# Performance work log

Hardware: AMD Instinct MI355X
Metric: run time of the kernel (lower is better)

The kernel has to match this reference:

```python
import jax, jax.numpy as jnp
import numpy as np

L, B, T, C, H, V = 6, 8, 1024, 1024, 16, 4096
HS = C // H  # head size = 64


def _ln(x, g, b):
    mu = x.mean(-1, keepdims=True)
    var = ((x - mu) ** 2).mean(-1, keepdims=True)
    return (x - mu) * jax.lax.rsqrt(var + 1e-5) * g + b


def setup_inputs() -> dict:
    key = jax.random.key(0)
    ks = jax.random.split(key, 12)
    s = 0.02
    return {
        "idx": jax.random.randint(ks[0], (B, T), 0, V),
        "tok_emb": jax.random.normal(ks[1], (V, C), jnp.float32) * s,
        "pos_emb": jax.random.normal(ks[2], (T, C), jnp.float32) * s,
        "Wq": jax.random.normal(ks[3], (L, C, C), jnp.float32) * s,
        "Wk": jax.random.normal(ks[4], (L, C, C), jnp.float32) * s,
        "Wv": jax.random.normal(ks[5], (L, C, C), jnp.float32) * s,
        "Wo": jax.random.normal(ks[6], (L, C, C), jnp.float32) * s,
        "bo": jnp.zeros((L, C), jnp.float32),
        "ln1_g": jnp.ones((L, C), jnp.float32),
        "ln1_b": jnp.zeros((L, C), jnp.float32),
        "ln2_g": jnp.ones((L, C), jnp.float32),
        "ln2_b": jnp.zeros((L, C), jnp.float32),
        "W1": jax.random.normal(ks[7], (L, C, 4 * C), jnp.float32) * s,
        "b1": jnp.zeros((L, 4 * C), jnp.float32),
        "W2": jax.random.normal(ks[8], (L, 4 * C, C), jnp.float32) * s,
        "b2": jnp.zeros((L, C), jnp.float32),
        "lnf_g": jnp.ones((C,), jnp.float32),
        "lnf_b": jnp.zeros((C,), jnp.float32),
        "lm_w": jax.random.normal(ks[9], (C, V), jnp.float32) * s,
        "lm_b": jnp.zeros((V,), jnp.float32),
    }


def _gpt(idx, tok_emb, pos_emb, Wq, Wk, Wv, Wo, bo, ln1_g, ln1_b, ln2_g, ln2_b,
         W1, b1, W2, b2, lnf_g, lnf_b, lm_w, lm_b):
    x = tok_emb[idx] + pos_emb[None, :idx.shape[1]]  # (B,T,C)
    mask = jnp.tril(jnp.ones((T, T), bool))
    neg_inf = jnp.float32(-jnp.inf)

    def block(x, p):
        wq, wk, wv, wo, bo_, g1, be1, g2, be2, w1, bb1, w2, bb2 = p
        h = _ln(x, g1, be1)
        # per-head projections (no bias), heads concatenated along feature dim
        q = (h @ wq).reshape(B, T, H, HS)
        k = (h @ wk).reshape(B, T, H, HS)
        v = (h @ wv).reshape(B, T, H, HS)
        # NOTE: faithful to source -- scores are MULTIPLIED by sqrt(head_size)
        att = jnp.einsum('bqhd,bkhd->bhqk', q, k) * (HS ** 0.5)
        att = jnp.where(mask, att, neg_inf)
        p_att = jax.nn.softmax(att, axis=-1)  # dropout is identity at eval
        o = jnp.einsum('bhqk,bkhd->bqhd', p_att, v).reshape(B, T, C)
        x = x + o @ wo + bo_
        h2 = _ln(x, g2, be2)
        x = x + jax.nn.relu(h2 @ w1 + bb1) @ w2 + bb2
        return x, None

    x, _ = jax.lax.scan(
        block, x,
        (Wq, Wk, Wv, Wo, bo, ln1_g, ln1_b, ln2_g, ln2_b, W1, b1, W2, b2))
    x = _ln(x, lnf_g, lnf_b)
    return x @ lm_w + lm_b  # logits (B,T,V)


def reference(idx, tok_emb, pos_emb, Wq, Wk, Wv, Wo, bo, ln1_g, ln1_b, ln2_g,
              ln2_b, W1, b1, W2, b2, lnf_g, lnf_b, lm_w, lm_b):
    return _gpt(idx, tok_emb, pos_emb, Wq, Wk, Wv, Wo, bo, ln1_g, ln1_b,
                ln2_g, ln2_b, W1, b1, W2, b2, lnf_g, lnf_b, lm_w, lm_b)
```

## Files before the change

### kernel.cpp

```cpp
#include <hip/hip_runtime.h>

#define LL 6
#define BB 8
#define TT 1024
#define CC 1024
#define HH 16
#define HS 64
#define VV 4096
#define BT (BB*TT)

typedef __attribute__((ext_vector_type(4))) float f32x4;
typedef __attribute__((ext_vector_type(8))) short bf16x8;

__device__ __forceinline__ float bf2f(unsigned short u) {
  union { unsigned int u; float f; } v; v.u = ((unsigned int)u) << 16; return v.f;
}
__device__ __forceinline__ unsigned short rne16(float f) {
  unsigned u = __float_as_uint(f);
  return (unsigned short)((u + 0x7fffu + ((u >> 16) & 1u)) >> 16);
}
__device__ __forceinline__ void gld16(const uint4* g, uint4* l) {
  __builtin_amdgcn_global_load_lds(
      (const __attribute__((address_space(1))) void*)g,
      (__attribute__((address_space(3))) void*)l, 16, 0, 0);
}

__global__ __launch_bounds__(256) void embed_kernel(
    const int* __restrict__ idx, const float* __restrict__ tok,
    const float* __restrict__ pos, float* __restrict__ x) {
  int bt = blockIdx.x;
  int t = bt & (TT - 1);
  int id = idx[bt];
  float4 te = reinterpret_cast<const float4*>(tok)[(size_t)id * (CC/4) + threadIdx.x];
  float4 pe = reinterpret_cast<const float4*>(pos)[(size_t)t * (CC/4) + threadIdx.x];
  float4 r; r.x = te.x+pe.x; r.y = te.y+pe.y; r.z = te.z+pe.z; r.w = te.w+pe.w;
  reinterpret_cast<float4*>(x)[(size_t)bt * (CC/4) + threadIdx.x] = r;
}

struct Oct3 { uint4 p0, p1, p2; };
__device__ __forceinline__ unsigned pk2(unsigned lo, unsigned hi) {
  return (lo >> 16) | (hi & 0xffff0000u);
}
__device__ __forceinline__ Oct3 split8(const float* f) {
  unsigned a0[8], a1[8], a2[8];
  #pragma unroll
  for (int e = 0; e < 8; ++e) {
    float v = f[e];
    unsigned u = __float_as_uint(v);
    a0[e] = u;
    float r = v - __uint_as_float(u & 0xffff0000u);
    unsigned ur = __float_as_uint(r);
    a1[e] = ur;
    float r2 = r - __uint_as_float(ur & 0xffff0000u);
    a2[e] = __float_as_uint(r2);
  }
  Oct3 o;
  o.p0 = make_uint4(pk2(a0[0],a0[1]), pk2(a0[2],a0[3]), pk2(a0[4],a0[5]), pk2(a0[6],a0[7]));
  o.p1 = make_uint4(pk2(a1[0],a1[1]), pk2(a1[2],a1[3]), pk2(a1[4],a1[5]), pk2(a1[6],a1[7]));
  o.p2 = make_uint4(pk2(a2[0],a2[1]), pk2(a2[2],a2[3]), pk2(a2[4],a2[5]), pk2(a2[6],a2[7]));
  return o;
}
struct Oct2 { uint4 p0, p1; };
__device__ __forceinline__ Oct2 split8_rne2(const float* f) {
  unsigned h0[8], h1[8];
  #pragma unroll
  for (int e = 0; e < 8; ++e) {
    h0[e] = rne16(f[e]);
    float r = f[e] - bf2f((unsigned short)h0[e]);
    h1[e] = rne16(r);
  }
  Oct2 o;
  o.p0 = make_uint4(h0[0]|(h0[1]<<16), h0[2]|(h0[3]<<16), h0[4]|(h0[5]<<16), h0[6]|(h0[7]<<16));
  o.p1 = make_uint4(h1[0]|(h1[1]<<16), h1[2]|(h1[3]<<16), h1[4]|(h1[5]<<16), h1[6]|(h1[7]<<16));
  return o;
}
__device__ __forceinline__ uint4 pack8_rne(const float* f) {
  unsigned h[8];
  #pragma unroll
  for (int e = 0; e < 8; ++e) h[e] = rne16(f[e]);
  return make_uint4(h[0]|(h[1]<<16), h[2]|(h[3]<<16), h[4]|(h[5]<<16), h[6]|(h[7]<<16));
}

__global__ __launch_bounds__(256) void ln32_kernel(
    const float* __restrict__ x, const float* __restrict__ g,
    const float* __restrict__ b, float* __restrict__ out) {
  __shared__ float red[8];
  int row = blockIdx.x, tid = threadIdx.x;
  float4 v = reinterpret_cast<const float4*>(x)[(size_t)row * (CC/4) + tid];
  float s  = v.x+v.y+v.z+v.w;
  float ss = v.x*v.x+v.y*v.y+v.z*v.z+v.w*v.w;
  #pragma unroll
  for (int off = 32; off; off >>= 1) { s += __shfl_xor(s, off); ss += __shfl_xor(ss, off); }
  if ((tid & 63) == 0) { red[tid>>6] = s; red[4+(tid>>6)] = ss; }
  __syncthreads();
  s  = red[0]+red[1]+red[2]+red[3];
  ss = red[4]+red[5]+red[6]+red[7];
  float mu = s * (1.f/CC);
  float rs = rsqrtf(ss*(1.f/CC) - mu*mu + 1e-5f);
  float4 gg = reinterpret_cast<const float4*>(g)[tid];
  float4 bb = reinterpret_cast<const float4*>(b)[tid];
  float4 o;
  o.x = (v.x-mu)*rs*gg.x + bb.x;
  o.y = (v.y-mu)*rs*gg.y + bb.y;
  o.z = (v.z-mu)*rs*gg.z + bb.z;
  o.w = (v.w-mu)*rs*gg.w + bb.w;
  reinterpret_cast<float4*>(out)[(size_t)row * (CC/4) + tid] = o;
}

__global__ __launch_bounds__(256) void lnsplit_kernel(
    const float* __restrict__ x, const float* __restrict__ g,
    const float* __restrict__ b, uint4* __restrict__ outp) {
  __shared__ float red[8];
  __shared__ float rowbuf[1024];
  int row = blockIdx.x, tid = threadIdx.x;
  float4 v = reinterpret_cast<const float4*>(x)[(size_t)row * (CC/4) + tid];
  float s  = v.x+v.y+v.z+v.w;
  float ss = v.x*v.x+v.y*v.y+v.z*v.z+v.w*v.w;
  #pragma unroll
  for (int off = 32; off; off >>= 1) { s += __shfl_xor(s, off); ss += __shfl_xor(ss, off); }
  if ((tid & 63) == 0) { red[tid>>6] = s; red[4+(tid>>6)] = ss; }
  __syncthreads();
  s  = red[0]+red[1]+red[2]+red[3];
  ss = red[4]+red[5]+red[6]+red[7];
  float mu = s * (1.f/CC);
  float rs = rsqrtf(ss*(1.f/CC) - mu*mu + 1e-5f);
  float4 gg = reinterpret_cast<const float4*>(g)[tid];
  float4 bb = reinterpret_cast<const float4*>(b)[tid];
  float4 o;
  o.x = (v.x-mu)*rs*gg.x + bb.x;
  o.y = (v.y-mu)*rs*gg.y + bb.y;
  o.z = (v.z-mu)*rs*gg.z + bb.z;
  o.w = (v.w-mu)*rs*gg.w + bb.w;
  *reinterpret_cast<float4*>(&rowbuf[tid*4]) = o;
  __syncthreads();
  if (tid < 128) {
    const size_t aPS = (size_t)128 * 16 * 512;
    int kt = tid >> 3, sl = tid & 7;
    int r = row & 63, mt = row >> 6;
    float f[8];
    #pragma unroll
    for (int e = 0; e < 8; ++e) f[e] = rowbuf[tid*8 + e];
    size_t di = ((size_t)(mt*16 + kt))*512 + r*8 + (sl ^ (r & 7));
    Oct2 ot = split8_rne2(f);
    outp[di] = ot.p0; outp[aPS+di] = ot.p1;
  }
}

__global__ __launch_bounds__(256) void bsplit4_kernel(
    const float* __restrict__ Wq, const float* __restrict__ Wk,
    const float* __restrict__ Wv, const float* __restrict__ Wo,
    uint4* __restrict__ bsQK, uint4* __restrict__ bsV, uint4* __restrict__ bsO) {
  int z = blockIdx.z;
  const float* Bw = (z == 0) ? Wq : (z == 1) ? Wk : (z == 2) ? Wv : Wo;
  uint4* outp = (z <= 1) ? bsQK : (z == 2) ? bsV : bsO;
  int ntile0 = (z == 1) ? 8 : 0;
  int ntTotal = (z <= 1) ? 16 : 8;
  int ntile = ntile0 + blockIdx.x, kt = blockIdx.y;
  size_t planeStride = (size_t)ntTotal * 16 * 1024;
  int tid = threadIdx.x;
  int bcol = tid & 127, bkcg = tid >> 7;
  #pragma unroll
  for (int g = 0; g < 4; ++g) {
    int kc = bkcg*4 + g;
    float f[8];
    #pragma unroll
    for (int j = 0; j < 8; ++j)
      f[j] = Bw[(size_t)(kt*64 + kc*8 + j) * CC + blockIdx.x*128 + bcol];
    size_t di = (((size_t)ntile * 16 + kt) * 8 + kc) * 128 + bcol;
    Oct2 o = split8_rne2(f);
    outp[di] = o.p0; outp[planeStride+di] = o.p1;
  }
}

template<int NP>
__global__ __launch_bounds__(256) void bsplit_kernel(
    const float* __restrict__ Bw, uint4* __restrict__ outp, int ldb,
    int ntile0, int ntTotal) {
  int ntile = ntile0 + blockIdx.x, kt = blockIdx.y;
  size_t planeStride = (size_t)ntTotal * gridDim.y * 1024;
  int tid = threadIdx.x;
  int bcol = tid & 127, bkcg = tid >> 7;
  #pragma unroll
  for (int g = 0; g < 4; ++g) {
    int kc = bkcg*4 + g;
    float f[8];
    #pragma unroll
    for (int j = 0; j < 8; ++j)
      f[j] = Bw[(size_t)(kt*64 + kc*8 + j) * ldb + blockIdx.x*128 + bcol];
    size_t di = (((size_t)ntile * gridDim.y + kt) * 8 + kc) * 128 + bcol;
    if (NP == 2) {
      Oct2 o = split8_rne2(f);
      outp[di] = o.p0; outp[planeStride+di] = o.p1;
    } else {
      outp[di] = pack8_rne(f);
    }
  }
}

template<int NP, bool ASP, int NM>
__global__ __launch_bounds__(256) void gemm128_kernel(
    const float* __restrict__ A, int lda,
    const uint4* __restrict__ Asp, size_t aPS,
    const uint4* __restrict__ Bs,
    const float* __restrict__ bias, const float* __restrict__ res,
    float* __restrict__ outf, int K, int ldc, int relu,
    int ntile0, int ntTotal, int kt0, int ktTotal, int vtmode,
    uint4* __restrict__ kout) {
  __shared__ uint4 lds_all[NP*2048];
  uint4* lds_a = lds_all;
  uint4* lds_b = lds_all + NP*1024;
  int tid = threadIdx.x;
  int by = blockIdx.y;
  int m0 = by * 128;
  int n0 = blockIdx.x * 128;
  int ntg = ntile0 + blockIdx.x;
  size_t bPS = (size_t)ntTotal * ktTotal * 1024;
  int lane = tid & 63, w = tid >> 6;
  int wm = w >> 1, wn = w & 1;
  int lr = lane & 15, lk = lane >> 4;
  int nkt = K >> 6;

  f32x4 acc[4][4];
  #pragma unroll
  for (int m = 0; m < 4; ++m)
    #pragma unroll
    for (int n = 0; n < 4; ++n)
      acc[m][n] = (f32x4){0.f, 0.f, 0.f, 0.f};

  for (int kt = 0; kt < nkt; ++kt) {
    if (ASP) {
      #pragma unroll
      for (int p = 0; p < NP; ++p) {
        const uint4* s0 = Asp + p*aPS + ((size_t)(2*by)   * nkt + kt)*512;
        const uint4* s1 = Asp + p*aPS + ((size_t)(2*by+1) * nkt + kt)*512;
        #pragma unroll
        for (int i = 0; i < 2; ++i) {
          int ch = w*2 + i;
          gld16(s0 + ch*64 + lane, &lds_a[p*1024 + ch*64]);
          gld16(s1 + ch*64 + lane, &lds_a[p*1024 + 512 + ch*64]);
        }
      }
    } else {
      #pragma unroll
      for (int i = 0; i < 4; ++i) {
        int c = tid + i * 256;
        int row = c >> 3, sl = c & 7;
        const float4* ap = reinterpret_cast<const float4*>(
            A + (size_t)(m0+row)*lda + kt*64 + sl*8);
        float4 x0 = ap[0], x1 = ap[1];
        float f[8] = {x0.x,x0.y,x0.z,x0.w,x1.x,x1.y,x1.z,x1.w};
        int di = (row>>6)*512 + (row&63)*8 + (sl ^ (row & 7));
        if (NP == 2) {
          Oct2 o = split8_rne2(f);
          lds_a[di] = o.p0; lds_a[1024 + di] = o.p1;
        } else {
          lds_a[di] = pack8_rne(f);
        }
      }
    }
    {
      int ktg = kt0 + kt;
      #pragma unroll
      for (int p = 0; p < NP; ++p) {
        const uint4* sb = Bs + p*bPS + ((size_t)ntg * ktTotal + ktg)*1024;
        #pragma unroll
        for (int i = 0; i < 4; ++i) {
          int ch = w*4 + i;
          gld16(sb + ch*64 + lane, &lds_b[p*1024 + ch*64]);
        }
      }
    }
    __syncthreads();
    #pragma unroll
    for (int ks = 0; ks < 2; ++ks) {
      int kc = ks*4 + lk;
      bf16x8 af[NP][4], bfr[NP][4];
      #pragma unroll
      for (int m = 0; m < 4; ++m) {
        int row = wm*64 + m*16 + lr;
        int si = (row>>6)*512 + (row&63)*8 + (kc ^ (row & 7));
        #pragma unroll
        for (int p = 0; p < NP; ++p)
          af[p][m] = reinterpret_cast<const bf16x8*>(lds_a + p*1024)[si];
      }
      #pragma unroll
      for (int n = 0; n < 4; ++n) {
        int si = kc*128 + wn*64 + n*16 + lr;
        #pragma unroll
        for (int p = 0; p < NP; ++p)
          bfr[p][n] = reinterpret_cast<const bf16x8*>(lds_b + p*1024)[si];
      }
      #pragma unroll
      for (int m = 0; m < 4; ++m)
        #pragma unroll
        for (int n = 0; n < 4; ++n) {
          acc[m][n] = __builtin_amdgcn_mfma_f32_16x16x32_bf16(af[0][m], bfr[0][n], acc[m][n], 0, 0, 0);
          if (NP == 2) {
            acc[m][n] = __builtin_amdgcn_mfma_f32_16x16x32_bf16(af[0][m], bfr[1][n], acc[m][n], 0, 0, 0);
            acc[m][n] = __builtin_amdgcn_mfma_f32_16x16x32_bf16(af[1][m], bfr[0][n], acc[m][n], 0, 0, 0);
            if (NM == 4)
              acc[m][n] = __builtin_amdgcn_mfma_f32_16x16x32_bf16(af[1][m], bfr[1][n], acc[m][n], 0, 0, 0);
          }
        }
    }
    __syncthreads();
  }

  if (vtmode == 1) {
    char* vb = (char*)outf;
    const size_t VPSb = (size_t)2048 * 512 * 16;
    #pragma unroll
    for (int m = 0; m < 4; ++m) {
      int row = m0 + wm*64 + m*16 + lk*4;
      int bq = row >> 10;
      int t  = row & (TT-1);
      int ktile = t >> 6, r = t & 63;
      int kc = r >> 3, toct0 = r & 7;
      #pragma unroll
      for (int n = 0; n < 4; ++n) {
        int col = n0 + wn*64 + n*16 + lr;
        int hh2 = col >> 6, d = col & 63;
        int tile = (bq*HH + hh2)*16 + ktile;
        int vi = kc*64 + ((d ^ (kc<<1)) & 63);
        unsigned p0[4], p1[4];
        #pragma unroll
        for (int j = 0; j < 4; ++j) {
          float v = acc[m][n][j];
          p0[j] = rne16(v);
          p1[j] = rne16(v - bf2f((unsigned short)p0[j]));
        }
        uint2 w0 = make_uint2(p0[0]|(p0[1]<<16), p0[2]|(p0[3]<<16));
        uint2 w1 = make_uint2(p1[0]|(p1[1]<<16), p1[2]|(p1[3]<<16));
        char* base = vb + ((size_t)tile*512 + vi)*16 + toct0*2;
        *reinterpret_cast<uint2*>(base) = w0;
        *reinterpret_cast<uint2*>(base + VPSb) = w1;
      }
    }
  } else if (vtmode == 2) {
    float* bounce = (float*)lds_all;
    #pragma unroll
    for (int m = 0; m < 4; ++m)
      #pragma unroll
      for (int n = 0; n < 4; ++n) {
        int cl = wn*64 + n*16 + lr;
        float bv = bias[n0 + cl];
        #pragma unroll
        for (int j = 0; j < 4; ++j) {
          int rl = wm*64 + m*16 + lk*4 + j;
          bounce[rl*128 + cl] = fmaxf(acc[m][n][j] + bv, 0.f);
        }
      }
    __syncthreads();
    uint4* a1p = (uint4*)outf;
    const size_t aPSa = (size_t)128 * 32 * 512;
    #pragma unroll
    for (int i = 0; i < 8; ++i) {
      int ot = tid + i*256;
      int r = ot >> 4, o = ot & 15;
      float f[8];
      #pragma unroll
      for (int e = 0; e < 8; ++e) f[e] = bounce[r*128 + o*8 + e];
      Oct2 o2 = split8_rne2(f);
      int mt = 2*by + (r>>6), rs = r & 63;
      int ktg = (n0 >> 6) + (o >> 3), sl = o & 7;
      size_t di = ((size_t)(mt*32 + ktg))*512 + rs*8 + (sl ^ (rs & 7));
      a1p[di] = o2.p0; a1p[aPSa + di] = o2.p1;
    }
  } else if (vtmode == 3 && ntg >= 8) {
    float* bounce = (float*)lds_all;
    #pragma unroll
    for (int m = 0; m < 4; ++m)
      #pragma unroll
      for (int n = 0; n < 4; ++n) {
        int cl = wn*64 + n*16 + lr;
        #pragma unroll
        for (int j = 0; j < 4; ++j) {
          int rl = wm*64 + m*16 + lk*4 + j;
          bounce[rl*128 + cl] = acc[m][n][j];
        }
      }
    __syncthreads();
    const size_t KPSC = (size_t)2048 * 512;
    int bq = m0 >> 10;
    int kt0tok = (m0 & 1023) >> 6;
    int hh0 = (ntg - 8) * 2;
    #pragma unroll
    for (int i = 0; i < 8; ++i) {
      int u = tid + i*256;
      int r = u >> 4, oct = u & 15;
      int head = oct >> 3, sl = oct & 7;
      float f[8];
      #pragma unroll
      for (int e = 0; e < 8; ++e) f[e] = bounce[r*128 + head*64 + sl*8 + e];
      Oct2 o = split8_rne2(f);
      int rk = r & 63;
      int tile = (bq*HH + hh0 + head)*16 + kt0tok + (r >> 6);
      size_t di = (size_t)tile*512 + rk*8 + (sl ^ (rk & 7));
      kout[di] = o.p0; kout[KPSC + di] = o.p1;
    }
  } else {
    #pragma unroll
    for (int m = 0; m < 4; ++m) {
      #pragma unroll
      for (int n = 0; n < 4; ++n) {
        int col = n0 + wn*64 + n*16 + lr;
        float bv = bias ? bias[col] : 0.f;
        #pragma unroll
        for (int j = 0; j < 4; ++j) {
          int row = m0 + wm*64 + m*16 + lk*4 + j;
          float vv = acc[m][n][j] + bv;
          if (relu) vv = fmaxf(vv, 0.f);
          size_t off = (size_t)row * ldc + col;
          if (res) vv += res[off];
          outf[off] = vv;
        }
      }
    }
  }
}

__global__ __launch_bounds__(256) void attn_mfma_kernel(
    const float* __restrict__ qf, const uint4* __restrict__ Kp,
    const uint4* __restrict__ Vp, uint4* __restrict__ aout) {
  __shared__ uint4 K_lds[2][512];
  __shared__ uint4 V_lds[2][512];
  __shared__ unsigned P_lds[64*68];
  const size_t KPS = (size_t)2048 * 512;
  const size_t VPS = (size_t)2048 * 512;
  const size_t APS = (size_t)128 * 16 * 512;
  int tid = threadIdx.x, lane = tid & 63, w = tid >> 6;
  int i = blockIdx.x;
  int xcd = i & 7, qm = (i >> 3) & 15, ghi = i >> 7;
  int g = ghi*8 + xcd;
  int b = g >> 4, hh = g & 15, qt = 15 - qm;
  int lr = lane & 15, lk = lane >> 4;
  const size_t tok0 = (size_t)b * TT;

  bf16x8 qa[2][2];
  {
    const float* qp = qf + (tok0 + qt*64 + w*16 + lr) * 1024 + hh*HS;
    #pragma unroll
    for (int ks = 0; ks < 2; ++ks) {
      const float4* p4 = reinterpret_cast<const float4*>(qp + ks*32 + lk*8);
      float4 a = p4[0], c = p4[1];
      float f[8] = {a.x,a.y,a.z,a.w,c.x,c.y,c.z,c.w};
      Oct2 ot = split8_rne2(f);
      qa[ks][0] = *reinterpret_cast<bf16x8*>(&ot.p0);
      qa[ks][1] = *reinterpret_cast<bf16x8*>(&ot.p1);
    }
  }

  float mrow[4] = {-3.0e38f,-3.0e38f,-3.0e38f,-3.0e38f};
  float lrow[4] = {0.f,0.f,0.f,0.f};
  f32x4 oac[4];
  #pragma unroll
  for (int n = 0; n < 4; ++n) oac[n] = (f32x4){0.f,0.f,0.f,0.f};

  for (int kt = 0; kt <= qt; ++kt) {
    __syncthreads();
    {
      int tile = ((b*HH + hh)*16 + kt);
      const uint4* ksrc = Kp + (size_t)tile*512;
      #pragma unroll
      for (int p = 0; p < 2; ++p)
        #pragma unroll
        for (int i2 = 0; i2 < 2; ++i2) {
          int ch = w*2 + i2;
          gld16(ksrc + p*KPS + ch*64 + lane, &K_lds[p][ch*64]);
        }
      const uint4* vsrc = Vp + (size_t)tile*512;
      #pragma unroll
      for (int p = 0; p < 2; ++p)
        #pragma unroll
        for (int i2 = 0; i2 < 2; ++i2) {
          int ch = w*2 + i2;
          gld16(vsrc + p*VPS + ch*64 + lane, &V_lds[p][ch*64]);
        }
    }
    __syncthreads();

    f32x4 sfr[4];
    #pragma unroll
    for (int nf = 0; nf < 4; ++nf) sfr[nf] = (f32x4){0.f,0.f,0.f,0.f};
    #pragma unroll
    for (int ks = 0; ks < 2; ++ks) {
      int kc = ks*4 + lk;
      #pragma unroll
      for (int nf = 0; nf < 4; ++nf) {
        int row = nf*16 + lr;
        int si = row*8 + (kc ^ (row & 7));
        bf16x8 k0 = *reinterpret_cast<const bf16x8*>(&K_lds[0][si]);
        bf16x8 k1 = *reinterpret_cast<const bf16x8*>(&K_lds[1][si]);
        sfr[nf] = __builtin_amdgcn_mfma_f32_16x16x32_bf16(qa[ks][0], k0, sfr[nf], 0,0,0);
        sfr[nf] = __builtin_amdgcn_mfma_f32_16x16x32_bf16(qa[ks][0], k1, sfr[nf], 0,0,0);
        sfr[nf] = __builtin_amdgcn_mfma_f32_16x16x32_bf16(qa[ks][1], k0, sfr[nf], 0,0,0);
      }
    }
    #pragma unroll
    for (int nf = 0; nf < 4; ++nf)
      #pragma unroll
      for (int j = 0; j < 4; ++j) {
        float s = sfr[nf][j] * 8.0f;
        if (kt == qt && (nf*16 + lr) > (w*16 + lk*4 + j)) s = -3.0e38f;
        sfr[nf][j] = s;
      }
    float alpha[4], tsum[4];
    #pragma unroll
    for (int j = 0; j < 4; ++j) {
      float mx = fmaxf(fmaxf(sfr[0][j], sfr[1][j]), fmaxf(sfr[2][j], sfr[3][j]));
      mx = fmaxf(mx, __shfl_xor(mx, 1));
      mx = fmaxf(mx, __shfl_xor(mx, 2));
      mx = fmaxf(mx, __shfl_xor(mx, 4));
      mx = fmaxf(mx, __shfl_xor(mx, 8));
      float mnew = fmaxf(mrow[j], mx);
      alpha[j] = __expf(mrow[j] - mnew);
      mrow[j] = mnew;
      tsum[j] = 0.f;
    }
    #pragma unroll
    for (int nf = 0; nf < 4; ++nf)
      #pragma unroll
      for (int j = 0; j < 4; ++j) {
        float p = __expf(sfr[nf][j] - mrow[j]);
        tsum[j] += p;
        unsigned u = __float_as_uint(p);
        float r = p - __uint_as_float(u & 0xffff0000u);
        unsigned pw = (u & 0xffff0000u) | (__float_as_uint(r) >> 16);
        int qrow = w*16 + lk*4 + j;
        int kcol = nf*16 + lr;
        P_lds[qrow*68 + (((kcol>>3) ^ (qrow & 7)))*8 + (kcol & 7)] = pw;
      }
    #pragma unroll
    for (int j = 0; j < 4; ++j) {
      float ts = tsum[j];
      ts += __shfl_xor(ts, 1);
      ts += __shfl_xor(ts, 2);
      ts += __shfl_xor(ts, 4);
      ts += __shfl_xor(ts, 8);
      lrow[j] = lrow[j]*alpha[j] + ts;
      oac[0][j] *= alpha[j]; oac[1][j] *= alpha[j];
      oac[2][j] *= alpha[j]; oac[3][j] *= alpha[j];
    }
    __syncthreads();

    #pragma unroll
    for (int ks = 0; ks < 2; ++ks) {
      int kc = ks*4 + lk;
      int prow = w*16 + lr;
      const uint4* pp4 = reinterpret_cast<const uint4*>(
          &P_lds[prow*68 + ((kc ^ (prow & 7)))*8]);
      uint4 pw0 = pp4[0], pw1 = pp4[1];
      uint4 phu, plu;
      phu.x = (pw0.x>>16) | (pw0.y & 0xffff0000u);
      phu.y = (pw0.z>>16) | (pw0.w & 0xffff0000u);
      phu.z = (pw1.x>>16) | (pw1.y & 0xffff0000u);
      phu.w = (pw1.z>>16) | (pw1.w & 0xffff0000u);
      plu.x = (pw0.x & 0xffffu) | (pw0.y << 16);
      plu.y = (pw0.z & 0xffffu) | (pw0.w << 16);
      plu.z = (pw1.x & 0xffffu) | (pw1.y << 16);
      plu.w = (pw1.z & 0xffffu) | (pw1.w << 16);
      bf16x8 ph = *reinterpret_cast<bf16x8*>(&phu);
      bf16x8 pl = *reinterpret_cast<bf16x8*>(&plu);
      #pragma unroll
      for (int nf2 = 0; nf2 < 4; ++nf2) {
        int d = nf2*16 + lr;
        int vi = kc*64 + ((d ^ (kc<<1)) & 63);
        bf16x8 vh = *reinterpret_cast<const bf16x8*>(&V_lds[0][vi]);
        bf16x8 vl = *reinterpret_cast<const bf16x8*>(&V_lds[1][vi]);
        oac[nf2] = __builtin_amdgcn_mfma_f32_16x16x32_bf16(ph, vh, oac[nf2], 0,0,0);
        oac[nf2] = __builtin_amdgcn_mfma_f32_16x16x32_bf16(ph, vl, oac[nf2], 0,0,0);
        oac[nf2] = __builtin_amdgcn_mfma_f32_16x16x32_bf16(pl, vh, oac[nf2], 0,0,0);
      }
    }
  }

  __syncthreads();
  float* Pf = (float*)P_lds;
  #pragma unroll
  for (int j = 0; j < 4; ++j) {
    float inv = 1.0f / lrow[j];
    #pragma unroll
    for (int nf2 = 0; nf2 < 4; ++nf2)
      Pf[(w*16 + lk*4 + j)*68 + nf2*16 + lr] = oac[nf2][j] * inv;
  }
  __syncthreads();
  int mtkt = (b*16 + qt)*16 + hh;
  #pragma unroll
  for (int i2 = 0; i2 < 2; ++i2) {
    int u = tid + i2*256;
    int r = u >> 3, sl = u & 7;
    float f[8];
    #pragma unroll
    for (int e = 0; e < 8; ++e) f[e] = Pf[r*68 + sl*8 + e];
    Oct2 o = split8_rne2(f);
    size_t di = (size_t)mtkt*512 + r*8 + (sl ^ (r & 7));
    aout[di] = o.p0; aout[APS + di] = o.p1;
  }
}

extern "C" void kernel_launch(void* const* d_in, const int* in_sizes, int n_in,
                              void* d_out, int out_size, void* d_ws, size_t ws_size,
                              hipStream_t stream) {
  const int*   idx  = (const int*)d_in[0];
  const float* tok  = (const float*)d_in[1];
  const float* pos  = (const float*)d_in[2];
  const float* Wq   = (const float*)d_in[3];
  const float* Wk   = (const float*)d_in[4];
  const float* Wv   = (const float*)d_in[5];
  const float* Wo   = (const float*)d_in[6];
  const float* bo   = (const float*)d_in[7];
  const float* ln1g = (const float*)d_in[8];
  const float* ln1b = (const float*)d_in[9];
  const float* ln2g = (const float*)d_in[10];
  const float* ln2b = (const float*)d_in[11];
  const float* W1   = (const float*)d_in[12];
  const float* b1   = (const float*)d_in[13];
  const float* W2   = (const float*)d_in[14];
  const float* b2   = (const float*)d_in[15];
  const float* lnfg = (const float*)d_in[16];
  const float* lnfb = (const float*)d_in[17];
  const float* lmw  = (const float*)d_in[18];
  const float* lmb  = (const float*)d_in[19];
  float* out = (float*)d_out;

  char* ob = (char*)d_out;
  float* x  = (float*)ob;
  float* vplanes = (float*)(ob + ((size_t)32<<20));
  float* qf = (float*)(ob + ((size_t)64<<20));
  uint4* Kp = (uint4*)(ob + ((size_t)96<<20));
  float* a1p = (float*)(ob + ((size_t)64<<20));
  char* wsb = (char*)d_ws;
  uint4* aspH  = (uint4*)wsb;
  uint4* bsQK  = (uint4*)(wsb + ((size_t)32<<20));
  uint4* bsV   = (uint4*)(wsb + ((size_t)40<<20));
  uint4* bsO   = (uint4*)(wsb + ((size_t)44<<20));
  uint4* aspH2 = (uint4*)wsb;
  uint4* aspH3 = (uint4*)wsb;
  uint4* bsW1  = (uint4*)(wsb + ((size_t)32<<20));
  uint4* bsW2  = (uint4*)(wsb + ((size_t)48<<20));
  float* hf    = (float*)wsb;
  uint4* bsL   = (uint4*)(wsb + ((size_t)32<<20));
  const size_t aPSh = (size_t)128 * 16 * 512;
  const size_t aPSa = (size_t)128 * 32 * 512;

  dim3 blk(256);
  dim3 gQK(16, 64), gV(8, 64), gO(8, 64);
  dim3 gW1(16, 64), gW2(8, 64), gL(32, 64);
  dim3 s4(8, 16, 4), sW1(32, 16), sW2(8, 64), sLM(32, 16);

  embed_kernel<<<BT, blk, 0, stream>>>(idx, tok, pos, x);
  for (int l = 0; l < LL; ++l) {
    const float* Wq_l = Wq + (size_t)l*CC*CC;
    const float* Wk_l = Wk + (size_t)l*CC*CC;
    const float* Wv_l = Wv + (size_t)l*CC*CC;
    const float* Wo_l = Wo + (size_t)l*CC*CC;
    const float* W1_l = W1 + (size_t)l*CC*4*CC;
    const float* W2_l = W2 + (size_t)l*4*CC*CC;
    lnsplit_kernel<<<BT, blk, 0, stream>>>(x, ln1g + (size_t)l*CC, ln1b + (size_t)l*CC, aspH);
    bsplit4_kernel<<<s4, blk, 0, stream>>>(Wq_l, Wk_l, Wv_l, Wo_l, bsQK, bsV, bsO);
    gemm128_kernel<2,true,4><<<gQK, blk, 0, stream>>>(nullptr, 0, aspH, aPSh, bsQK,
        nullptr, nullptr, qf, CC, 1024, 0, 0, 16, 0, 16, 3, Kp);
    gemm128_kernel<2,true,3><<<gV, blk, 0, stream>>>(nullptr, 0, aspH, aPSh, bsV,
        nullptr, nullptr, vplanes, CC, CC, 0, 0, 8, 0, 16, 1, nullptr);
    attn_mfma_kernel<<<BB*HH*16, blk, 0, stream>>>(qf, Kp, (const uint4*)vplanes, aspH2);
    gemm128_kernel<2,true,3><<<gO, blk, 0, stream>>>(nullptr, 0, aspH2, aPSh, bsO,
        bo + (size_t)l*CC, x, x, CC, CC, 0, 0, 8, 0, 16, 0, nullptr);
    lnsplit_kernel<<<BT, blk, 0, stream>>>(x, ln2g + (size_t)l*CC, ln2b + (size_t)l*CC, aspH3);
    bsplit_kernel<2><<<sW1, blk, 0, stream>>>(W1_l, bsW1, 4*CC, 0, 32);
    bsplit_kernel<2><<<sW2, blk, 0, stream>>>(W2_l, bsW2, CC, 0, 8);
    gemm128_kernel<2,true,3><<<gW1, blk, 0, stream>>>(nullptr, 0, aspH3, aPSh, bsW1,
        b1 + (size_t)l*4*CC, nullptr, a1p, CC, 2048, 1, 0, 32, 0, 16, 2, nullptr);
    gemm128_kernel<2,true,3><<<gW2, blk, 0, stream>>>(nullptr, 0, (const uint4*)a1p, aPSa, bsW2,
        b2 + (size_t)l*CC, x, x, 2048, CC, 0, 0, 8, 0, 64, 0, nullptr);
    gemm128_kernel<2,true,3><<<gW1, blk, 0, stream>>>(nullptr, 0, aspH3, aPSh, bsW1,
        b1 + (size_t)l*4*CC + 2048, nullptr, a1p, CC, 2048, 1, 16, 32, 0, 16, 2, nullptr);
    gemm128_kernel<2,true,3><<<gW2, blk, 0, stream>>>(nullptr, 0, (const uint4*)a1p, aPSa, bsW2,
        nullptr, x, x, 2048, CC, 0, 0, 8, 32, 64, 0, nullptr);
  }
  ln32_kernel<<<BT, blk, 0, stream>>>(x, lnfg, lnfb, hf);
  bsplit_kernel<1><<<sLM, blk, 0, stream>>>(lmw, bsL, VV, 0, 32);
  gemm128_kernel<1,false,1><<<gL, blk, 0, stream>>>(hf, CC, nullptr, 0, bsL,
      lmb, nullptr, out, CC, VV, 0, 0, 32, 0, 16, 0, nullptr);
}
```

Baseline: 4.720 ms.

## Remap GEMM block indices per XCD and pre-pack final LN output as bf16

The GEMM kernel now remaps its linear block id so blocks dispatched to the same XCD (round-robin over eight) share M-tiles and reuse the same A rows in that die's L2. The final layernorm now writes a pre-swizzled single-plane bf16 A operand, and the LM-head GEMM switches to the pre-split A path instead of converting fp32 activations inside the GEMM. This aims to cut L2 misses and in-loop conversion work. The remap assumes gridDim.y is a multiple of 8, which holds for all launches here.

```diff
diff --git a/kernel.cpp b/kernel.cpp
--- a/kernel.cpp
+++ b/kernel.cpp
@@ -37,29 +37,6 @@
   reinterpret_cast<float4*>(x)[(size_t)bt * (CC/4) + threadIdx.x] = r;
 }
 
-struct Oct3 { uint4 p0, p1, p2; };
-__device__ __forceinline__ unsigned pk2(unsigned lo, unsigned hi) {
-  return (lo >> 16) | (hi & 0xffff0000u);
-}
-__device__ __forceinline__ Oct3 split8(const float* f) {
-  unsigned a0[8], a1[8], a2[8];
-  #pragma unroll
-  for (int e = 0; e < 8; ++e) {
-    float v = f[e];
-    unsigned u = __float_as_uint(v);
-    a0[e] = u;
-    float r = v - __uint_as_float(u & 0xffff0000u);
-    unsigned ur = __float_as_uint(r);
-    a1[e] = ur;
-    float r2 = r - __uint_as_float(ur & 0xffff0000u);
-    a2[e] = __float_as_uint(r2);
-  }
-  Oct3 o;
-  o.p0 = make_uint4(pk2(a0[0],a0[1]), pk2(a0[2],a0[3]), pk2(a0[4],a0[5]), pk2(a0[6],a0[7]));
-  o.p1 = make_uint4(pk2(a1[0],a1[1]), pk2(a1[2],a1[3]), pk2(a1[4],a1[5]), pk2(a1[6],a1[7]));
-  o.p2 = make_uint4(pk2(a2[0],a2[1]), pk2(a2[2],a2[3]), pk2(a2[4],a2[5]), pk2(a2[6],a2[7]));
-  return o;
-}
 struct Oct2 { uint4 p0, p1; };
 __device__ __forceinline__ Oct2 split8_rne2(const float* f) {
   unsigned h0[8], h1[8];
@@ -79,32 +56,6 @@
   #pragma unroll
   for (int e = 0; e < 8; ++e) h[e] = rne16(f[e]);
   return make_uint4(h[0]|(h[1]<<16), h[2]|(h[3]<<16), h[4]|(h[5]<<16), h[6]|(h[7]<<16));
-}
-
-__global__ __launch_bounds__(256) void ln32_kernel(
-    const float* __restrict__ x, const float* __restrict__ g,
-    const float* __restrict__ b, float* __restrict__ out) {
-  __shared__ float red[8];
-  int row = blockIdx.x, tid = threadIdx.x;
-  float4 v = reinterpret_cast<const float4*>(x)[(size_t)row * (CC/4) + tid];
-  float s  = v.x+v.y+v.z+v.w;
-  float ss = v.x*v.x+v.y*v.y+v.z*v.z+v.w*v.w;
-  #pragma unroll
-  for (int off = 32; off; off >>= 1) { s += __shfl_xor(s, off); ss += __shfl_xor(ss, off); }
-  if ((tid & 63) == 0) { red[tid>>6] = s; red[4+(tid>>6)] = ss; }
-  __syncthreads();
-  s  = red[0]+red[1]+red[2]+red[3];
-  ss = red[4]+red[5]+red[6]+red[7];
-  float mu = s * (1.f/CC);
-  float rs = rsqrtf(ss*(1.f/CC) - mu*mu + 1e-5f);
-  float4 gg = reinterpret_cast<const float4*>(g)[tid];
-  float4 bb = reinterpret_cast<const float4*>(b)[tid];
-  float4 o;
-  o.x = (v.x-mu)*rs*gg.x + bb.x;
-  o.y = (v.y-mu)*rs*gg.y + bb.y;
-  o.z = (v.z-mu)*rs*gg.z + bb.z;
-  o.w = (v.w-mu)*rs*gg.w + bb.w;
-  reinterpret_cast<float4*>(out)[(size_t)row * (CC/4) + tid] = o;
 }
 
 __global__ __launch_bounds__(256) void lnsplit_kernel(
@@ -146,6 +97,43 @@
   }
 }
 
+__global__ __launch_bounds__(256) void lnsplit1_kernel(
+    const float* __restrict__ x, const float* __restrict__ g,
+    const float* __restrict__ b, uint4* __restrict__ outp) {
+  __shared__ float red[8];
+  __shared__ float rowbuf[1024];
+  int row = blockIdx.x, tid = threadIdx.x;
+  float4 v = reinterpret_cast<const float4*>(x)[(size_t)row * (CC/4) + tid];
+  float s  = v.x+v.y+v.z+v.w;
+  float ss = v.x*v.x+v.y*v.y+v.z*v.z+v.w*v.w;
+  #pragma unroll
+  for (int off = 32; off; off >>= 1) { s += __shfl_xor(s, off); ss += __shfl_xor(ss, off); }
+  if ((tid & 63) == 0) { red[tid>>6] = s; red[4+(tid>>6)] = ss; }
+  __syncthreads();
+  s  = red[0]+red[1]+red[2]+red[3];
+  ss = red[4]+red[5]+red[6]+red[7];
+  float mu = s * (1.f/CC);
+  float rs = rsqrtf(ss*(1.f/CC) - mu*mu + 1e-5f);
+  float4 gg = reinterpret_cast<const float4*>(g)[tid];
+  float4 bb = reinterpret_cast<const float4*>(b)[tid];
+  float4 o;
+  o.x = (v.x-mu)*rs*gg.x + bb.x;
+  o.y = (v.y-mu)*rs*gg.y + bb.y;
+  o.z = (v.z-mu)*rs*gg.z + bb.z;
+  o.w = (v.w-mu)*rs*gg.w + bb.w;
+  *reinterpret_cast<float4*>(&rowbuf[tid*4]) = o;
+  __syncthreads();
+  if (tid < 128) {
+    int kt = tid >> 3, sl = tid & 7;
+    int r = row & 63, mt = row >> 6;
+    float f[8];
+    #pragma unroll
+    for (int e = 0; e < 8; ++e) f[e] = rowbuf[tid*8 + e];
+    size_t di = ((size_t)(mt*16 + kt))*512 + r*8 + (sl ^ (r & 7));
+    outp[di] = pack8_rne(f);
+  }
+}
+
 __global__ __launch_bounds__(256) void bsplit4_kernel(
     const float* __restrict__ Wq, const float* __restrict__ Wk,
     const float* __restrict__ Wv, const float* __restrict__ Wo,
@@ -210,10 +198,14 @@
   uint4* lds_a = lds_all;
   uint4* lds_b = lds_all + NP*1024;
   int tid = threadIdx.x;
-  int by = blockIdx.y;
+  int NYd8 = gridDim.y >> 3;
+  int li = blockIdx.x + gridDim.x * blockIdx.y;
+  int xcd = li & 7, j = li >> 3;
+  int by = xcd + 8 * (j % NYd8);
+  int bx = j / NYd8;
   int m0 = by * 128;
-  int n0 = blockIdx.x * 128;
-  int ntg = ntile0 + blockIdx.x;
+  int n0 = bx * 128;
+  int ntg = ntile0 + bx;
   size_t bPS = (size_t)ntTotal * ktTotal * 1024;
   int lane = tid & 63, w = tid >> 6;
   int wm = w >> 1, wn = w & 1;
@@ -324,10 +316,10 @@
         int vi = kc*64 + ((d ^ (kc<<1)) & 63);
         unsigned p0[4], p1[4];
         #pragma unroll
-        for (int j = 0; j < 4; ++j) {
-          float v = acc[m][n][j];
-          p0[j] = rne16(v);
-          p1[j] = rne16(v - bf2f((unsigned short)p0[j]));
+        for (int j2 = 0; j2 < 4; ++j2) {
+          float v = acc[m][n][j2];
+          p0[j2] = rne16(v);
+          p1[j2] = rne16(v - bf2f((unsigned short)p0[j2]));
         }
         uint2 w0 = make_uint2(p0[0]|(p0[1]<<16), p0[2]|(p0[3]<<16));
         uint2 w1 = make_uint2(p1[0]|(p1[1]<<16), p1[2]|(p1[3]<<16));
@@ -345,9 +337,9 @@
         int cl = wn*64 + n*16 + lr;
         float bv = bias[n0 + cl];
         #pragma unroll
-        for (int j = 0; j < 4; ++j) {
-          int rl = wm*64 + m*16 + lk*4 + j;
-          bounce[rl*128 + cl] = fmaxf(acc[m][n][j] + bv, 0.f);
+        for (int j2 = 0; j2 < 4; ++j2) {
+          int rl = wm*64 + m*16 + lk*4 + j2;
+          bounce[rl*128 + cl] = fmaxf(acc[m][n][j2] + bv, 0.f);
         }
       }
     __syncthreads();
@@ -374,9 +366,9 @@
       for (int n = 0; n < 4; ++n) {
         int cl = wn*64 + n*16 + lr;
         #pragma unroll
-        for (int j = 0; j < 4; ++j) {
-          int rl = wm*64 + m*16 + lk*4 + j;
-          bounce[rl*128 + cl] = acc[m][n][j];
+        for (int j2 = 0; j2 < 4; ++j2) {
+          int rl = wm*64 + m*16 + lk*4 + j2;
+          bounce[rl*128 + cl] = acc[m][n][j2];
         }
       }
     __syncthreads();
@@ -406,9 +398,9 @@
         int col = n0 + wn*64 + n*16 + lr;
         float bv = bias ? bias[col] : 0.f;
         #pragma unroll
-        for (int j = 0; j < 4; ++j) {
-          int row = m0 + wm*64 + m*16 + lk*4 + j;
-          float vv = acc[m][n][j] + bv;
+        for (int j2 = 0; j2 < 4; ++j2) {
+          int row = m0 + wm*64 + m*16 + lk*4 + j2;
+          float vv = acc[m][n][j2] + bv;
           if (relu) vv = fmaxf(vv, 0.f);
           size_t off = (size_t)row * ldc + col;
           if (res) vv += res[off];
@@ -638,7 +630,7 @@
   uint4* aspH3 = (uint4*)wsb;
   uint4* bsW1  = (uint4*)(wsb + ((size_t)32<<20));
   uint4* bsW2  = (uint4*)(wsb + ((size_t)48<<20));
-  float* hf    = (float*)wsb;
+  uint4* hfp   = (uint4*)wsb;
   uint4* bsL   = (uint4*)(wsb + ((size_t)32<<20));
   const size_t aPSh = (size_t)128 * 16 * 512;
   const size_t aPSa = (size_t)128 * 32 * 512;
@@ -677,8 +669,8 @@
     gemm128_kernel<2,true,3><<<gW2, blk, 0, stream>>>(nullptr, 0, (const uint4*)a1p, aPSa, bsW2,
         nullptr, x, x, 2048, CC, 0, 0, 8, 32, 64, 0, nullptr);
   }
-  ln32_kernel<<<BT, blk, 0, stream>>>(x, lnfg, lnfb, hf);
+  lnsplit1_kernel<<<BT, blk, 0, stream>>>(x, lnfg, lnfb, hfp);
   bsplit_kernel<1><<<sLM, blk, 0, stream>>>(lmw, bsL, VV, 0, 32);
-  gemm128_kernel<1,false,1><<<gL, blk, 0, stream>>>(hf, CC, nullptr, 0, bsL,
+  gemm128_kernel<1,true,1><<<gL, blk, 0, stream>>>(nullptr, 0, hfp, aPSh, bsL,
       lmb, nullptr, out, CC, VV, 0, 0, 32, 0, 16, 0, nullptr);
 }
```

Measured after the change: 4.392 ms. -6.9%, faster.
